# Performance work log

Hardware: AMD Instinct MI355X
Metric: run time of the kernel (lower is better)

Reference implementation:

```python
import jax, jax.numpy as jnp
import numpy as np

DIM = 192
HEADS = 4
EPS = 1e-12  # F.normalize default eps


def setup_inputs() -> dict:
    key = jax.random.key(0)
    k0, k1, k2, k3 = jax.random.split(key, 4)
    x = jax.random.normal(k0, (4, DIM, 128, 128), dtype=jnp.float32)
    # qkv 1x1 conv weight: [3*dim, dim, 1, 1] -> stored as [3*dim, dim]
    w_qkv = jax.random.normal(k1, (3 * DIM, DIM), dtype=jnp.float32) * (1.0 / np.sqrt(DIM))
    # depthwise 3x3 conv weight: [3*dim, 1, 3, 3]
    w_dw = jax.random.normal(k2, (3 * DIM, 1, 3, 3), dtype=jnp.float32) * (1.0 / 3.0)
    # project_out 1x1 conv weight: [dim, dim]
    w_proj = jax.random.normal(k3, (DIM, DIM), dtype=jnp.float32) * (1.0 / np.sqrt(DIM))
    # temperature: ones(heads,1,1), requires_grad=False in original
    temperature = jnp.ones((HEADS, 1, 1), dtype=jnp.float32)
    return {"x": x, "w_qkv": w_qkv, "w_dw": w_dw, "w_proj": w_proj,
            "temperature": temperature}


def _l2norm(t):
    # F.normalize(t, dim=-1): t / max(||t||_2, eps)
    n = jnp.sqrt(jnp.sum(t * t, axis=-1, keepdims=True))
    return t / jnp.maximum(n, EPS)


def reference(x, w_qkv, w_dw, w_proj, temperature):
    b, c, h, w = x.shape
    ch = c // HEADS  # channels per head
    # 1x1 conv (no bias) == channel GEMM
    qkv = jnp.einsum('oc,bchw->bohw', w_qkv, x)
    # depthwise 3x3 conv, padding=1, groups=3*dim
    qkv = jax.lax.conv_general_dilated(
        qkv, w_dw, window_strides=(1, 1), padding=((1, 1), (1, 1)),
        dimension_numbers=('NCHW', 'OIHW', 'NCHW'),
        feature_group_count=3 * c)
    q, k, v = jnp.split(qkv, 3, axis=1)
    # b (head ch) h w -> b head ch (h w)
    def rearr(t):
        return t.reshape(b, HEADS, ch, h * w)
    q, k, v = rearr(q), rearr(k), rearr(v)
    q = _l2norm(q)
    k = _l2norm(k)
    # channel-channel attention: [b, head, ch, ch]
    attn = jnp.einsum('bhcn,bhdn->bhcd', q, k) * temperature[None]
    attn = jax.nn.softmax(attn, axis=-1)
    out = jnp.einsum('bhcd,bhdn->bhcn', attn, v)
    out = out.reshape(b, c, h, w)
    out = jnp.einsum('oc,bchw->bohw', w_proj, out)
    return out
```

## Files before the change

### kernel.cpp

```cpp
#include <hip/hip_runtime.h>

typedef unsigned short u16;
typedef float f32x4 __attribute__((ext_vector_type(4)));
typedef __bf16 bf16x8 __attribute__((ext_vector_type(8)));
typedef unsigned short u16x8 __attribute__((ext_vector_type(8)));
typedef unsigned short u16x4 __attribute__((ext_vector_type(4)));

#define DEV static __device__ __forceinline__

DEV u16 f2bf(float f) {
  unsigned int u = __float_as_uint(f);
  u += 0x7FFFu + ((u >> 16) & 1u);
  return (u16)(u >> 16);
}
DEV float bf2f(u16 h) { return __uint_as_float(((unsigned int)h) << 16); }

DEV void gload_lds16(const void* g, void* l) {
  __builtin_amdgcn_global_load_lds(
      (__attribute__((address_space(1))) void*)(unsigned long long)g,
      (__attribute__((address_space(3))) void*)l, 16, 0, 0);
}

__global__ __launch_bounds__(256) void convert_w_pack_kernel(
    const float* __restrict__ w, u16* __restrict__ out) {
  const int t = blockIdx.x * 256 + threadIdx.x;
  const int lane = t & 63, chunk = t >> 6;
  const int ks = chunk % 6, r = chunk / 6;
  const int nj = r & 1, wn = (r >> 1) & 1, j = r >> 2;
  const int row = j * 64 + wn * 32 + nj * 16 + (lane & 15);
  const int ke = ks * 32 + (lane >> 4) * 8;
  const f32x4 a = *(const f32x4*)(w + row * 192 + ke);
  const f32x4 c = *(const f32x4*)(w + row * 192 + ke + 4);
  u16x8 o;
  o[0] = f2bf(a.x); o[1] = f2bf(a.y); o[2] = f2bf(a.z); o[3] = f2bf(a.w);
  o[4] = f2bf(c.x); o[5] = f2bf(c.y); o[6] = f2bf(c.z); o[7] = f2bf(c.w);
  *(u16x8*)(out + (size_t)t * 8) = o;
}

template <bool IN_F32, bool OUT_BF16, int NJ>
__global__ __launch_bounds__(256) void gemm_bt_kernel(
    const void* __restrict__ Av, const u16* __restrict__ Bpack,
    void* __restrict__ Cv, size_t aBatch, size_t bBatch, size_t cBatch,
    int ldC) {
  __shared__ __align__(16) char sA[24576];

  const int tid = threadIdx.x, wave = tid >> 6, lane = tid & 63;
  const int id = blockIdx.x;
  const int m0 = (id & 255) * 64, b = id >> 8;
  const u16* Bp = Bpack + (size_t)b * bBatch;

  if (IN_F32) {
    const float* Xb = (const float*)Av + (size_t)b * aBatch + m0;
    const int cbl = tid & 15, iq = tid >> 4;
    f32x4 vaf[3][4];
#pragma unroll
    for (int p = 0; p < 3; ++p)
#pragma unroll
      for (int r = 0; r < 4; ++r)
        vaf[p][r] = *(const f32x4*)(Xb + (size_t)((p * 16 + cbl) * 4 + r) *
                                             16384 + iq * 4);
#pragma unroll
    for (int p = 0; p < 3; ++p) {
      const int cb = p * 16 + cbl;
#pragma unroll
      for (int j = 0; j < 4; ++j) {
        const int n = iq * 4 + j;
        u16x4 col;
        col[0] = f2bf(vaf[p][0][j]);
        col[1] = f2bf(vaf[p][1][j]);
        col[2] = f2bf(vaf[p][2][j]);
        col[3] = f2bf(vaf[p][3][j]);
        *(u16x4*)(sA + n * 384 + ((cb * 8) ^ ((n & 7) << 4))) = col;
      }
    }
  } else {
    const u16* Vb = (const u16*)Av + (size_t)b * aBatch + m0;
    u16x8 vau[2][4];
#pragma unroll
    for (int p = 0; p < 2; ++p) {
      const int task = p * 256 + tid;
      if (task < 384) {
        const int cb = task >> 3, io = task & 7;
#pragma unroll
        for (int r = 0; r < 4; ++r)
          vau[p][r] = *(const u16x8*)(Vb + (size_t)(cb * 4 + r) * 16384 +
                                      io * 8);
      }
    }
#pragma unroll
    for (int p = 0; p < 2; ++p) {
      const int task = p * 256 + tid;
      if (task < 384) {
        const int cb = task >> 3, io = task & 7;
#pragma unroll
        for (int j = 0; j < 8; ++j) {
          const int n = io * 8 + j;
          u16x4 col;
          col[0] = vau[p][0][j];
          col[1] = vau[p][1][j];
          col[2] = vau[p][2][j];
          col[3] = vau[p][3][j];
          *(u16x4*)(sA + n * 384 + ((cb * 8) ^ ((n & 7) << 4))) = col;
        }
      }
    }
  }
  __syncthreads();

  const int wm = wave & 1, wn = wave >> 1;
  const int l15 = lane & 15, lg = lane >> 4;
  const int swm = (l15 & 7) << 4;
  const int rA0 = (wm * 32 + l15) * 384;

  bf16x8 af[2][6];
#pragma unroll
  for (int mi = 0; mi < 2; ++mi)
#pragma unroll
    for (int ks = 0; ks < 6; ++ks)
      af[mi][ks] = *(const bf16x8*)(sA + rA0 + mi * 16 * 384 +
                                    ((ks * 64 + lg * 16) ^ swm));

#pragma unroll
  for (int j = 0; j < NJ; ++j) {
    bf16x8 bfv[2][6];
#pragma unroll
    for (int nj = 0; nj < 2; ++nj)
#pragma unroll
      for (int ks = 0; ks < 6; ++ks)
        bfv[nj][ks] = *(const bf16x8*)(
            Bp + ((size_t)((j * 4 + wn * 2 + nj) * 6 + ks) * 512) + lane * 8);
    f32x4 acc[2][2];
#pragma unroll
    for (int mi = 0; mi < 2; ++mi)
#pragma unroll
      for (int nj = 0; nj < 2; ++nj) acc[mi][nj] = (f32x4){0.f, 0.f, 0.f, 0.f};
#pragma unroll
    for (int ks = 0; ks < 6; ++ks)
#pragma unroll
      for (int mi = 0; mi < 2; ++mi)
#pragma unroll
        for (int nj = 0; nj < 2; ++nj)
          acc[mi][nj] = __builtin_amdgcn_mfma_f32_16x16x32_bf16(
              af[mi][ks], bfv[nj][ks], acc[mi][nj], 0, 0, 0);
    const int j0 = j * 64;
    if (OUT_BF16) {
      u16* Cb = (u16*)Cv + (size_t)b * cBatch;
#pragma unroll
      for (int mi = 0; mi < 2; ++mi)
#pragma unroll
        for (int nj = 0; nj < 2; ++nj) {
          u16x4 ov;
#pragma unroll
          for (int r = 0; r < 4; ++r) ov[r] = f2bf(acc[mi][nj][r]);
          *(u16x4*)(Cb + (size_t)(j0 + wn * 32 + nj * 16 + l15) * ldC + m0 +
                    wm * 32 + mi * 16 + lg * 4) = ov;
        }
    } else {
      float* Cb = (float*)Cv + (size_t)b * cBatch;
#pragma unroll
      for (int mi = 0; mi < 2; ++mi)
#pragma unroll
        for (int nj = 0; nj < 2; ++nj)
          *(f32x4*)(Cb + (size_t)(j0 + wn * 32 + nj * 16 + l15) * ldC + m0 +
                    wm * 32 + mi * 16 + lg * 4) = acc[mi][nj];
    }
  }
}

__global__ __launch_bounds__(256) void dwconv_kernel(
    u16* __restrict__ qkv, const float* __restrict__ wdw,
    float* __restrict__ sq) {
  __shared__ u16 img[16384];
  __shared__ float red[4];
  const int o = blockIdx.x, b = blockIdx.y;
  const size_t base = ((size_t)b * 576 + o) * 16384;
  const int tid = threadIdx.x, wave = tid >> 6, lane = tid & 63;
#pragma unroll
  for (int i = 0; i < 8; ++i) {
    const int off = (i * 4 + wave) * 1024;
    gload_lds16((const char*)qkv + base * 2 + off + lane * 16, (char*)img + off);
  }
  asm volatile("s_waitcnt vmcnt(0)" ::: "memory");
  __syncthreads();
  float w[9];
#pragma unroll
  for (int j = 0; j < 9; ++j) w[j] = wdw[o * 9 + j];
  float sqacc = 0.f;
  for (int it = 0; it < 8; ++it) {
    const int chunk = it * 256 + tid;
    const int px0 = chunk * 8;
    const int y = px0 >> 7, x0 = px0 & 127;
    float acc[8];
#pragma unroll
    for (int j = 0; j < 8; ++j) acc[j] = 0.f;
#pragma unroll
    for (int dy = -1; dy <= 1; ++dy) {
      const int yy = y + dy;
      float v[10];
      if (yy >= 0 && yy <= 127) {
        const u16* rowp = img + yy * 128 + x0;
        u16x8 m = *(const u16x8*)rowp;
#pragma unroll
        for (int j = 0; j < 8; ++j) v[j + 1] = bf2f(m[j]);
        v[0] = (x0 > 0) ? bf2f(rowp[-1]) : 0.f;
        v[9] = (x0 < 120) ? bf2f(rowp[8]) : 0.f;
      } else {
#pragma unroll
        for (int j = 0; j < 10; ++j) v[j] = 0.f;
      }
      const float w0 = w[(dy + 1) * 3], w1 = w[(dy + 1) * 3 + 1],
                  w2 = w[(dy + 1) * 3 + 2];
#pragma unroll
      for (int j = 0; j < 8; ++j) acc[j] += w0 * v[j] + w1 * v[j + 1] + w2 * v[j + 2];
    }
    u16x8 ov;
#pragma unroll
    for (int j = 0; j < 8; ++j) {
      sqacc += acc[j] * acc[j];
      ov[j] = f2bf(acc[j]);
    }
    *(u16x8*)(qkv + base + px0) = ov;
  }
#pragma unroll
  for (int s = 32; s > 0; s >>= 1) sqacc += __shfl_xor(sqacc, s, 64);
  if (lane == 0) red[wave] = sqacc;
  __syncthreads();
  if (tid == 0) sq[b * 576 + o] = red[0] + red[1] + red[2] + red[3];
}

__global__ __launch_bounds__(256) void gram_kernel(
    const u16* __restrict__ qkv, float* __restrict__ partial) {
  __shared__ u16 tiles[4 * 3072];
  __shared__ float red[4 * 2304];
  const int bh = blockIdx.y, b = bh >> 2, h = bh & 3;
  const int g = blockIdx.x;
  const int wave = threadIdx.x >> 6, lane = threadIdx.x & 63;
  const int n0 = g * 512 + wave * 128;
  const u16* qb = qkv + ((size_t)b * 576 + h * 48) * 16384;
  const u16* kb = qb + (size_t)192 * 16384;
  char* tl = (char*)(tiles + wave * 3072);
  const int l15 = lane & 15, lg = lane >> 4;
  const int swz = (l15 & 3) << 4;
  f32x4 acc[3][3];
#pragma unroll
  for (int i = 0; i < 3; ++i)
#pragma unroll
    for (int j = 0; j < 3; ++j) acc[i][j] = (f32x4){0.f, 0.f, 0.f, 0.f};

  for (int ks = 0; ks < 4; ++ks) {
    const int nn = n0 + ks * 32;
    asm volatile("s_waitcnt lgkmcnt(0)" ::: "memory");
#pragma unroll
    for (int i = 0; i < 6; ++i) {
      const int flat = i * 1024 + lane * 16;
      const int row = flat >> 6, colb = flat & 63;
      const u16* src = (row < 48) ? (qb + (size_t)row * 16384 + nn)
                                  : (kb + (size_t)(row - 48) * 16384 + nn);
      gload_lds16((const char*)src + (colb ^ ((row & 3) << 4)), tl + i * 1024);
    }
    asm volatile("s_waitcnt vmcnt(0)" ::: "memory");
    bf16x8 qf[3], kf[3];
#pragma unroll
    for (int f = 0; f < 3; ++f) {
      qf[f] = *(const bf16x8*)(tl + (f * 16 + l15) * 64 + ((lg * 16) ^ swz));
      kf[f] = *(const bf16x8*)(tl + (48 + f * 16 + l15) * 64 + ((lg * 16) ^ swz));
    }
#pragma unroll
    for (int i = 0; i < 3; ++i)
#pragma unroll
      for (int j = 0; j < 3; ++j)
        acc[i][j] = __builtin_amdgcn_mfma_f32_16x16x32_bf16(qf[i], kf[j],
                                                            acc[i][j], 0, 0, 0);
  }
  {
    float* rw = red + wave * 2304;
#pragma unroll
    for (int i = 0; i < 3; ++i)
#pragma unroll
      for (int j = 0; j < 3; ++j)
#pragma unroll
        for (int r = 0; r < 4; ++r)
          rw[(i * 16 + lg * 4 + r) * 48 + (j * 16 + l15)] = acc[i][j][r];
  }
  __syncthreads();
#pragma unroll
  for (int it = 0; it < 9; ++it) {
    const int p = it * 256 + threadIdx.x;
    const float s = red[p] + red[2304 + p] + red[4608 + p] + red[6912 + p];
    partial[((size_t)bh * 2304 + p) * 32 + g] = s;
  }
}

__global__ __launch_bounds__(256) void reduce_partial_kernel(
    const float* __restrict__ partial, float* __restrict__ G) {
  const int idx = blockIdx.x * 256 + threadIdx.x;
  const f32x4* pp = (const f32x4*)(partial + (size_t)idx * 32);
  const f32x4 a = (pp[0] + pp[1]) + (pp[2] + pp[3]) +
                  (pp[4] + pp[5]) + (pp[6] + pp[7]);
  G[idx] = a.x + a.y + a.z + a.w;
}

__global__ __launch_bounds__(256) void softmax_weff_kernel(
    const float* __restrict__ Gin, const float* __restrict__ sq,
    const float* __restrict__ temp, const float* __restrict__ wproj,
    u16* __restrict__ weff) {
  __shared__ float G[2304];
  __shared__ float wp[192 * 49];
  __shared__ float nq[48], nk[48];
  const int bh = blockIdx.x, b = bh >> 2, h = bh & 3;
  const int tid = threadIdx.x;
#pragma unroll
  for (int it = 0; it < 36; ++it) {
    const int j = it * 256 + tid;
    const int o = j / 48, c = j - o * 48;
    wp[o * 49 + c] = wproj[o * 192 + h * 48 + c];
  }
#pragma unroll
  for (int it = 0; it < 9; ++it) {
    const int p = it * 256 + tid;
    G[p] = Gin[(size_t)bh * 2304 + p];
  }
  if (tid < 48) {
    nq[tid] = fmaxf(sqrtf(sq[b * 576 + h * 48 + tid]), 1e-12f);
    nk[tid] = fmaxf(sqrtf(sq[b * 576 + 192 + h * 48 + tid]), 1e-12f);
  }
  __syncthreads();
  if (tid < 48) {
    const int r = tid;
    const float inq = temp[h] / nq[r];
    float L[48];
    float mx = -3.4e38f;
#pragma unroll 4
    for (int d = 0; d < 48; ++d) {
      const float v = G[r * 48 + d] * inq / nk[d];
      L[d] = v;
      mx = fmaxf(mx, v);
    }
    float s = 0.f;
#pragma unroll 4
    for (int d = 0; d < 48; ++d) {
      const float e = __expf(L[d] - mx);
      L[d] = e;
      s += e;
    }
    const float inv = 1.f / s;
#pragma unroll 4
    for (int d = 0; d < 48; ++d) G[r * 48 + d] = L[d] * inv;
  }
  __syncthreads();
  if (tid < 192) {
    const int o = tid;
    f32x4 acc[12];
#pragma unroll
    for (int dv = 0; dv < 12; ++dv) acc[dv] = (f32x4){0.f, 0.f, 0.f, 0.f};
    for (int c = 0; c < 48; ++c) {
      const float w = wp[o * 49 + c];
      const f32x4* at = (const f32x4*)(G + c * 48);
#pragma unroll
      for (int dv = 0; dv < 12; ++dv) acc[dv] += w * at[dv];
    }
    u16* op = weff + (size_t)b * 36864;
    const int jj = o >> 6, wn = (o >> 5) & 1, nj = (o >> 4) & 1, l15 = o & 15;
#pragma unroll
    for (int g8 = 0; g8 < 6; ++g8) {
      const int c2 = h * 48 + g8 * 8;
      const int ks = c2 >> 5, lg = (c2 >> 3) & 3;
      u16x8 ov;
#pragma unroll
      for (int q = 0; q < 8; ++q) {
        const int d = g8 * 8 + q;
        ov[q] = f2bf(acc[d >> 2][d & 3]);
      }
      *(u16x8*)(op + ((size_t)((jj * 4 + wn * 2 + nj) * 6 + ks) * 512) +
                (lg * 16 + l15) * 8) = ov;
    }
  }
}

extern "C" void kernel_launch(void* const* d_in, const int* in_sizes, int n_in,
                              void* d_out, int out_size, void* d_ws,
                              size_t ws_size, hipStream_t stream) {
  (void)in_sizes; (void)n_in; (void)out_size; (void)ws_size;
  const float* x      = (const float*)d_in[0];
  const float* w_qkv  = (const float*)d_in[1];
  const float* w_dw   = (const float*)d_in[2];
  const float* w_proj = (const float*)d_in[3];
  const float* temp   = (const float*)d_in[4];

  char* ws = (char*)d_ws;
  u16*   qkv     = (u16*)ws;
  float* partial = (float*)(ws + 75497472);
  float* G       = (float*)(ws + 80216064);
  float* sq      = (float*)(ws + 80363520);
  u16*   Wq      = (u16*)(ws + 80372736);
  u16*   Weff    = (u16*)(ws + 80593920);

  convert_w_pack_kernel<<<dim3(54), 256, 0, stream>>>(w_qkv, Wq);
  gemm_bt_kernel<true, true, 9><<<dim3(1024), 256, 0, stream>>>(
      x, Wq, qkv, (size_t)192 * 16384, 0, (size_t)576 * 16384, 16384);
  dwconv_kernel<<<dim3(576, 4), 256, 0, stream>>>(qkv, w_dw, sq);
  gram_kernel<<<dim3(32, 16), 256, 0, stream>>>(qkv, partial);
  reduce_partial_kernel<<<dim3(144), 256, 0, stream>>>(partial, G);
  softmax_weff_kernel<<<dim3(16), 256, 0, stream>>>(G, sq, temp, w_proj, Weff);
  gemm_bt_kernel<false, false, 3><<<dim3(1024), 256, 0, stream>>>(
      qkv + (size_t)384 * 16384, Weff, d_out, (size_t)576 * 16384,
      (size_t)36864, (size_t)192 * 16384, 16384);
}
```

Baseline: 141.4 us.

## Stage weight tiles in LDS and enlarge GEMM block tile to 128x192

The channel GEMM now uses 512-thread blocks that each compute a 128-pixel by 192-output-channel tile. The weight slice is copied into swizzled LDS with direct global-to-LDS loads, instead of each wave re-reading pre-packed fragments from global memory across several output sub-tiles. The weight packing kernel becomes a plain bf16 conversion, and the fused projection weights are written row-major to match. This aims to raise operand reuse and cut repeated global traffic for B. In exchange it uses about 120KB of LDS per block, which limits occupancy to one block per CU, and it needs more accumulator registers per wave.

After: 151.4 us. 7.1% more time.

```diff
diff --git a/kernel.cpp b/kernel.cpp
--- a/kernel.cpp
+++ b/kernel.cpp
@@ -21,33 +21,35 @@
       (__attribute__((address_space(3))) void*)l, 16, 0, 0);
 }
 
-__global__ __launch_bounds__(256) void convert_w_pack_kernel(
-    const float* __restrict__ w, u16* __restrict__ out) {
-  const int t = blockIdx.x * 256 + threadIdx.x;
-  const int lane = t & 63, chunk = t >> 6;
-  const int ks = chunk % 6, r = chunk / 6;
-  const int nj = r & 1, wn = (r >> 1) & 1, j = r >> 2;
-  const int row = j * 64 + wn * 32 + nj * 16 + (lane & 15);
-  const int ke = ks * 32 + (lane >> 4) * 8;
-  const f32x4 a = *(const f32x4*)(w + row * 192 + ke);
-  const f32x4 c = *(const f32x4*)(w + row * 192 + ke + 4);
-  u16x8 o;
-  o[0] = f2bf(a.x); o[1] = f2bf(a.y); o[2] = f2bf(a.z); o[3] = f2bf(a.w);
-  o[4] = f2bf(c.x); o[5] = f2bf(c.y); o[6] = f2bf(c.z); o[7] = f2bf(c.w);
-  *(u16x8*)(out + (size_t)t * 8) = o;
-}
-
-template <bool IN_F32, bool OUT_BF16, int NJ>
-__global__ __launch_bounds__(256) void gemm_bt_kernel(
-    const void* __restrict__ Av, const u16* __restrict__ Bpack,
+__global__ __launch_bounds__(256) void convert_w_kernel(
+    const float* __restrict__ in, u16* __restrict__ out, int n) {
+  int i = blockIdx.x * 256 + threadIdx.x;
+  if (i < n) out[i] = f2bf(in[i]);
+}
+
+template <bool IN_F32, bool OUT_BF16>
+__global__ __launch_bounds__(512, 2) void gemm_bt_kernel(
+    const void* __restrict__ Av, const u16* __restrict__ B,
     void* __restrict__ Cv, size_t aBatch, size_t bBatch, size_t cBatch,
     int ldC) {
-  __shared__ __align__(16) char sA[24576];
+  __shared__ __align__(16) char smem[122880];
+  char* sA = smem;
+  char* sB = smem + 49152;
 
   const int tid = threadIdx.x, wave = tid >> 6, lane = tid & 63;
-  const int id = blockIdx.x;
-  const int m0 = (id & 255) * 64, b = id >> 8;
-  const u16* Bp = Bpack + (size_t)b * bBatch;
+  const int m0 = blockIdx.x * 128;
+  const int jg = blockIdx.y, b = blockIdx.z;
+
+  const char* Bbase = (const char*)(B + (size_t)b * bBatch);
+#pragma unroll
+  for (int i = 0; i < 9; ++i) {
+    const int c = i * 8 + wave;
+    const int d = c * 1024 + lane * 16;
+    const int row = d / 384, inrow = d - row * 384;
+    gload_lds16(Bbase + (size_t)(jg * 192 + row) * 384 +
+                    (inrow ^ ((row & 7) << 4)),
+                sB + c * 1024);
+  }
 
   if (IN_F32) {
     const float* Xb = (const float*)Av + (size_t)b * aBatch + m0;
@@ -75,95 +77,85 @@
     }
   } else {
     const u16* Vb = (const u16*)Av + (size_t)b * aBatch + m0;
-    u16x8 vau[2][4];
 #pragma unroll
     for (int p = 0; p < 2; ++p) {
-      const int task = p * 256 + tid;
-      if (task < 384) {
-        const int cb = task >> 3, io = task & 7;
+      const int task = p * 512 + tid;
+      if (task < 768) {
+        const int cb = task >> 4, io = task & 15;
+        u16x8 v[4];
 #pragma unroll
         for (int r = 0; r < 4; ++r)
-          vau[p][r] = *(const u16x8*)(Vb + (size_t)(cb * 4 + r) * 16384 +
-                                      io * 8);
-      }
-    }
-#pragma unroll
-    for (int p = 0; p < 2; ++p) {
-      const int task = p * 256 + tid;
-      if (task < 384) {
-        const int cb = task >> 3, io = task & 7;
+          v[r] = *(const u16x8*)(Vb + (size_t)(cb * 4 + r) * 16384 + io * 8);
 #pragma unroll
         for (int j = 0; j < 8; ++j) {
           const int n = io * 8 + j;
           u16x4 col;
-          col[0] = vau[p][0][j];
-          col[1] = vau[p][1][j];
-          col[2] = vau[p][2][j];
-          col[3] = vau[p][3][j];
+          col[0] = v[0][j];
+          col[1] = v[1][j];
+          col[2] = v[2][j];
+          col[3] = v[3][j];
           *(u16x4*)(sA + n * 384 + ((cb * 8) ^ ((n & 7) << 4))) = col;
         }
       }
     }
   }
-  __syncthreads();
-
-  const int wm = wave & 1, wn = wave >> 1;
+  asm volatile("s_waitcnt vmcnt(0) lgkmcnt(0)" ::: "memory");
+  __syncthreads();
+
+  const int wm = wave >> 1, wn = wave & 1;
   const int l15 = lane & 15, lg = lane >> 4;
   const int swm = (l15 & 7) << 4;
-  const int rA0 = (wm * 32 + l15) * 384;
 
   bf16x8 af[2][6];
 #pragma unroll
   for (int mi = 0; mi < 2; ++mi)
 #pragma unroll
     for (int ks = 0; ks < 6; ++ks)
-      af[mi][ks] = *(const bf16x8*)(sA + rA0 + mi * 16 * 384 +
+      af[mi][ks] = *(const bf16x8*)(sA + (wm * 32 + mi * 16 + l15) * 384 +
                                     ((ks * 64 + lg * 16) ^ swm));
 
-#pragma unroll
-  for (int j = 0; j < NJ; ++j) {
-    bf16x8 bfv[2][6];
-#pragma unroll
-    for (int nj = 0; nj < 2; ++nj)
-#pragma unroll
-      for (int ks = 0; ks < 6; ++ks)
-        bfv[nj][ks] = *(const bf16x8*)(
-            Bp + ((size_t)((j * 4 + wn * 2 + nj) * 6 + ks) * 512) + lane * 8);
-    f32x4 acc[2][2];
+  f32x4 acc[2][6];
+#pragma unroll
+  for (int mi = 0; mi < 2; ++mi)
+#pragma unroll
+    for (int nj = 0; nj < 6; ++nj) acc[mi][nj] = (f32x4){0.f, 0.f, 0.f, 0.f};
+
+#pragma unroll
+  for (int ks = 0; ks < 6; ++ks) {
+    bf16x8 bfv[6];
+#pragma unroll
+    for (int nj = 0; nj < 6; ++nj)
+      bfv[nj] = *(const bf16x8*)(sB + (wn * 96 + nj * 16 + l15) * 384 +
+                                 ((ks * 64 + lg * 16) ^ swm));
 #pragma unroll
     for (int mi = 0; mi < 2; ++mi)
 #pragma unroll
-      for (int nj = 0; nj < 2; ++nj) acc[mi][nj] = (f32x4){0.f, 0.f, 0.f, 0.f};
-#pragma unroll
-    for (int ks = 0; ks < 6; ++ks)
-#pragma unroll
-      for (int mi = 0; mi < 2; ++mi)
-#pragma unroll
-        for (int nj = 0; nj < 2; ++nj)
-          acc[mi][nj] = __builtin_amdgcn_mfma_f32_16x16x32_bf16(
-              af[mi][ks], bfv[nj][ks], acc[mi][nj], 0, 0, 0);
-    const int j0 = j * 64;
-    if (OUT_BF16) {
-      u16* Cb = (u16*)Cv + (size_t)b * cBatch;
-#pragma unroll
-      for (int mi = 0; mi < 2; ++mi)
-#pragma unroll
-        for (int nj = 0; nj < 2; ++nj) {
-          u16x4 ov;
-#pragma unroll
-          for (int r = 0; r < 4; ++r) ov[r] = f2bf(acc[mi][nj][r]);
-          *(u16x4*)(Cb + (size_t)(j0 + wn * 32 + nj * 16 + l15) * ldC + m0 +
-                    wm * 32 + mi * 16 + lg * 4) = ov;
-        }
-    } else {
-      float* Cb = (float*)Cv + (size_t)b * cBatch;
-#pragma unroll
-      for (int mi = 0; mi < 2; ++mi)
-#pragma unroll
-        for (int nj = 0; nj < 2; ++nj)
-          *(f32x4*)(Cb + (size_t)(j0 + wn * 32 + nj * 16 + l15) * ldC + m0 +
-                    wm * 32 + mi * 16 + lg * 4) = acc[mi][nj];
-    }
+      for (int nj = 0; nj < 6; ++nj)
+        acc[mi][nj] = __builtin_amdgcn_mfma_f32_16x16x32_bf16(
+            af[mi][ks], bfv[nj], acc[mi][nj], 0, 0, 0);
+  }
+
+  const int orow0 = jg * 192 + wn * 96;
+  if (OUT_BF16) {
+    u16* Cb = (u16*)Cv + (size_t)b * cBatch;
+#pragma unroll
+    for (int mi = 0; mi < 2; ++mi)
+#pragma unroll
+      for (int nj = 0; nj < 6; ++nj) {
+        u16x4 ov;
+#pragma unroll
+        for (int r = 0; r < 4; ++r) ov[r] = f2bf(acc[mi][nj][r]);
+        *(u16x4*)(Cb + (size_t)(orow0 + nj * 16 + l15) * ldC + m0 + wm * 32 +
+                  mi * 16 + lg * 4) = ov;
+      }
+  } else {
+    float* Cb = (float*)Cv + (size_t)b * cBatch;
+#pragma unroll
+    for (int mi = 0; mi < 2; ++mi)
+#pragma unroll
+      for (int nj = 0; nj < 6; ++nj)
+        *(f32x4*)(Cb + (size_t)(orow0 + nj * 16 + l15) * ldC + m0 + wm * 32 +
+                  mi * 16 + lg * 4) = acc[mi][nj];
   }
 }
 
@@ -359,20 +351,16 @@
 #pragma unroll
       for (int dv = 0; dv < 12; ++dv) acc[dv] += w * at[dv];
     }
-    u16* op = weff + (size_t)b * 36864;
-    const int jj = o >> 6, wn = (o >> 5) & 1, nj = (o >> 4) & 1, l15 = o & 15;
+    u16* op = weff + ((size_t)b * 192 + o) * 192 + h * 48;
 #pragma unroll
     for (int g8 = 0; g8 < 6; ++g8) {
-      const int c2 = h * 48 + g8 * 8;
-      const int ks = c2 >> 5, lg = (c2 >> 3) & 3;
       u16x8 ov;
 #pragma unroll
-      for (int q = 0; q < 8; ++q) {
-        const int d = g8 * 8 + q;
-        ov[q] = f2bf(acc[d >> 2][d & 3]);
-      }
-      *(u16x8*)(op + ((size_t)((jj * 4 + wn * 2 + nj) * 6 + ks) * 512) +
-                (lg * 16 + l15) * 8) = ov;
+      for (int j = 0; j < 8; ++j) {
+        const int d = g8 * 8 + j;
+        ov[j] = f2bf(acc[d >> 2][d & 3]);
+      }
+      *(u16x8*)(op + g8 * 8) = ov;
     }
   }
 }
@@ -395,14 +383,14 @@
   u16*   Wq      = (u16*)(ws + 80372736);
   u16*   Weff    = (u16*)(ws + 80593920);
 
-  convert_w_pack_kernel<<<dim3(54), 256, 0, stream>>>(w_qkv, Wq);
-  gemm_bt_kernel<true, true, 9><<<dim3(1024), 256, 0, stream>>>(
+  convert_w_kernel<<<dim3(432), 256, 0, stream>>>(w_qkv, Wq, 110592);
+  gemm_bt_kernel<true, true><<<dim3(128, 3, 4), 512, 0, stream>>>(
       x, Wq, qkv, (size_t)192 * 16384, 0, (size_t)576 * 16384, 16384);
   dwconv_kernel<<<dim3(576, 4), 256, 0, stream>>>(qkv, w_dw, sq);
   gram_kernel<<<dim3(32, 16), 256, 0, stream>>>(qkv, partial);
   reduce_partial_kernel<<<dim3(144), 256, 0, stream>>>(partial, G);
   softmax_weff_kernel<<<dim3(16), 256, 0, stream>>>(G, sq, temp, w_proj, Weff);
-  gemm_bt_kernel<false, false, 3><<<dim3(1024), 256, 0, stream>>>(
+  gemm_bt_kernel<false, false><<<dim3(128, 1, 4), 512, 0, stream>>>(
       qkv + (size_t)384 * 16384, Weff, d_out, (size_t)576 * 16384,
-      (size_t)36864, (size_t)192 * 16384, 16384);
-}
+      (size_t)192 * 192, (size_t)192 * 16384, 16384);
+}
```
